# Performance work log

Hardware: AMD Instinct MI355X
Metric: run time of the kernel (lower is better)

## Reference

```python
import jax, jax.numpy as jnp
import numpy as np

D = 768
ED = 192  # d // 4
E = 8     # n_experts
K = 2     # top_k
B, H, W = 32, 32, 32
LN_EPS = 1e-5


def setup_inputs() -> dict:
    key = jax.random.key(0)
    ks = jax.random.split(key, 5)
    s = 0.02
    x = jax.random.normal(ks[0], (B, D, H, W), dtype=jnp.float32)
    Wr = jax.random.normal(ks[1], (E, D), dtype=jnp.float32) * s   # router: logits = tokens @ Wr.T
    W1 = jax.random.normal(ks[2], (E, D, ED), dtype=jnp.float32) * s  # gate proj (silu branch)
    W3 = jax.random.normal(ks[3], (E, D, ED), dtype=jnp.float32) * s  # linear branch
    W2 = jax.random.normal(ks[4], (E, ED, D), dtype=jnp.float32) * s  # down proj
    gamma = jnp.ones((D,), dtype=jnp.float32)
    beta = jnp.zeros((D,), dtype=jnp.float32)
    return {"x": x, "Wr": Wr, "W1": W1, "W3": W3, "W2": W2, "gamma": gamma, "beta": beta}


def _layernorm(y, gamma, beta):
    mu = jnp.mean(y, axis=-1, keepdims=True)
    var = jnp.mean(jnp.square(y - mu), axis=-1, keepdims=True)
    return (y - mu) * jax.lax.rsqrt(var + LN_EPS) * gamma + beta


def _moe_forward(x, Wr, W1, W3, W2, gamma, beta):
    b, c, h, w = x.shape
    tokens = x.transpose(0, 2, 3, 1).reshape(-1, c)        # [T, d]
    logits = tokens @ Wr.T                                  # [T, E]
    topk_v, topk_i = jax.lax.top_k(logits, K)               # [T, K]
    topk_w = jax.nn.softmax(topk_v, axis=-1)                # [T, K]
    # dense combine weights: zero for non-selected experts (same math as masked scatter)
    gates = jnp.sum(jax.nn.one_hot(topk_i, E, dtype=tokens.dtype) * topk_w[..., None], axis=1)  # [T, E]
    # SwiGLU per expert (forward uses silu(e[0](t)) * e[2](t), then e[3])
    hdn = jax.nn.silu(jnp.einsum('td,edh->teh', tokens, W1)) * jnp.einsum('td,edh->teh', tokens, W3)  # [T,E,ed]
    y = jnp.einsum('te,teh,ehd->td', gates, hdn, W2)        # combine: [T, d]
    out = _layernorm(y, gamma, beta) + tokens
    return out.reshape(b, h, w, c).transpose(0, 3, 1, 2)


def reference(x, Wr, W1, W3, W2, gamma, beta):
    return _moe_forward(x, Wr, W1, W3, W2, gamma, beta)
```

## Files before the change

### kernel.cpp

```cpp
#include <hip/hip_runtime.h>
#include <cstdint>
#include <cstddef>

#define T_TOK 32768
#define DM 768
#define EDIM 192
#define NEXP 8

typedef unsigned short u16;
typedef short bf16x8 __attribute__((ext_vector_type(8)));
typedef float f32x4 __attribute__((ext_vector_type(4)));
typedef u16 u16x8 __attribute__((ext_vector_type(8)));

__device__ __forceinline__ u16 f2bf(float f) {
  unsigned u = __float_as_uint(f);
  return (u16)((u + 0x7FFFu + ((u >> 16) & 1u)) >> 16);
}
__device__ __forceinline__ float bf2f(u16 u) {
  return __uint_as_float(((unsigned)u) << 16);
}

__device__ __forceinline__ void gld16(const void* g, void* l) {
  __builtin_amdgcn_global_load_lds(
      (const __attribute__((address_space(1))) unsigned int*)g,
      (__attribute__((address_space(3))) unsigned int*)l,
      16, 0, 0);
}

__device__ __forceinline__ bf16x8 frag_ld(const u16* lds, int row, int kb) {
  int ph = row * 128 + (kb ^ ((row & 7) << 4));
  return *(const bf16x8*)((const char*)lds + ph);
}

__global__ __launch_bounds__(256) void k_prep(
    const float* __restrict__ W1, const float* __restrict__ W3,
    const float* __restrict__ W2, u16* __restrict__ W1T,
    u16* __restrict__ W3T, u16* __restrict__ W2T)
{
  __shared__ __align__(16) float td[64][68];
  const int z = blockIdx.z;
  const int mat = z >> 3, e = z & 7;
  const int R = (mat == 2) ? EDIM : DM;
  const int C = (mat == 2) ? DM : EDIM;
  const int r0 = blockIdx.x * 64, c0 = blockIdx.y * 64;
  if (r0 >= R || c0 >= C) return;
  const float* in = (mat == 0 ? W1 : mat == 1 ? W3 : W2) + (size_t)e * R * C;
  u16* out = (mat == 0 ? W1T : mat == 1 ? W3T : W2T) + (size_t)e * R * C;
  const int tid = threadIdx.x;
  {
    int rl = tid >> 2, cs = (tid & 3) * 16;
    const float* s = in + (size_t)(r0 + rl) * C + c0 + cs;
    #pragma unroll
    for (int i = 0; i < 16; i += 4) *(float4*)&td[rl][cs + i] = *(const float4*)(s + i);
  }
  __syncthreads();
  {
    int cl = tid >> 2, rs = (tid & 3) * 16;
    u16* d = out + (size_t)(c0 + cl) * R + r0 + rs;
    u16x8 o0, o1;
    #pragma unroll
    for (int i = 0; i < 8; ++i) {
      o0[i] = f2bf(td[rs + i][cl]);
      o1[i] = f2bf(td[rs + 8 + i][cl]);
    }
    *(u16x8*)d = o0;
    *(u16x8*)(d + 8) = o1;
  }
}

__global__ __launch_bounds__(256) void k_tokrouter(
    const float* __restrict__ x, const float* __restrict__ Wr,
    u16* __restrict__ tokbf, int* __restrict__ cnt,
    int* __restrict__ toklist, float* __restrict__ gatelist)
{
  __shared__ float WrL[8][772];
  __shared__ float xL[64][33];
  __shared__ float logitsL[32][8];
  __shared__ int cnt8[8];
  __shared__ int baseL[8];
  const int tid = threadIdx.x;
  const int t0 = blockIdx.x * 32;
  const int b = t0 >> 10;
  const int h = (t0 >> 5) & 31;
  const float* xb = x + (size_t)b * (DM * 1024) + h * 32;

  for (int i = tid; i < 1536; i += 256) {
    int r = i / 192;
    int c = (i - r * 192) * 4;
    *(float4*)&WrL[r][c] = ((const float4*)Wr)[i];
  }

  const int rt = tid >> 3;
  const int re = tid & 7;
  float lacc = 0.f;

  for (int cb = 0; cb < 12; ++cb) {
    const int c0 = cb * 64;
    __syncthreads();
    #pragma unroll
    for (int it = 0; it < 2; ++it) {
      int idx = it * 256 + tid;
      int r = idx >> 3, cc = (idx & 7) * 4;
      float4 v = *(const float4*)(xb + (size_t)(c0 + r) * 1024 + cc);
      xL[r][cc] = v.x; xL[r][cc + 1] = v.y; xL[r][cc + 2] = v.z; xL[r][cc + 3] = v.w;
    }
    __syncthreads();
    {
      const float* wr = &WrL[re][c0];
      #pragma unroll
      for (int c = 0; c < 64; ++c) lacc = fmaf(xL[c][rt], wr[c], lacc);
    }
    {
      u16x8 o;
      #pragma unroll
      for (int i = 0; i < 8; ++i) o[i] = f2bf(xL[re * 8 + i][rt]);
      *(u16x8*)(tokbf + (size_t)(t0 + rt) * DM + c0 + re * 8) = o;
    }
  }

  logitsL[rt][re] = lacc;
  if (tid < 8) cnt8[tid] = 0;
  __syncthreads();

  int e0 = -1, e1 = -1, lp0 = 0, lp1 = 0;
  float g0 = 0.f, g1 = 0.f;
  if (tid < 32) {
    float v0 = -1e30f, v1 = -1e30f;
    #pragma unroll
    for (int e = 0; e < 8; ++e) { float v = logitsL[tid][e]; if (v > v0) { v0 = v; e0 = e; } }
    #pragma unroll
    for (int e = 0; e < 8; ++e) {
      if (e == e0) continue;
      float v = logitsL[tid][e]; if (v > v1) { v1 = v; e1 = e; }
    }
    float w = expf(v1 - v0);
    g0 = 1.f / (1.f + w);
    g1 = w / (1.f + w);
    lp0 = atomicAdd(&cnt8[e0], 1);
    lp1 = atomicAdd(&cnt8[e1], 1);
  }
  __syncthreads();
  if (tid < 8) baseL[tid] = atomicAdd(&cnt[tid], cnt8[tid]);
  __syncthreads();
  if (tid < 32) {
    int tg = t0 + tid;
    int p0 = baseL[e0] + lp0;
    int p1 = baseL[e1] + lp1;
    toklist[e0 * T_TOK + p0] = tg;
    gatelist[e0 * T_TOK + p0] = g0;
    toklist[e1 * T_TOK + p1] = tg | (1 << 16);
    gatelist[e1 * T_TOK + p1] = g1;
  }
}

__global__ void k_prefix(const int* __restrict__ cnt, int* __restrict__ offs) {
  if (threadIdx.x == 0) {
    int s = 0;
    for (int e = 0; e < NEXP; ++e) { offs[e] = s; s += cnt[e]; }
    offs[NEXP] = s;
  }
}

__global__ __launch_bounds__(256) void k_ffn1(
    const u16* __restrict__ tokbf, const u16* __restrict__ W1T,
    const u16* __restrict__ W3T, const int* __restrict__ cnt,
    const int* __restrict__ offs, const int* __restrict__ toklist,
    u16* __restrict__ hbuf)
{
  __shared__ __align__(16) u16 As[128 * 64];
  __shared__ __align__(16) u16 B1s[64 * 64];
  __shared__ __align__(16) u16 B3s[64 * 64];
  __shared__ int rowbaseL[128];
  const int e = blockIdx.z;
  const int count = cnt[e];
  const int start = blockIdx.x * 128;
  if (start >= count) return;
  const int n0 = blockIdx.y * 64;
  const int rows = min(128, count - start);
  const int tid = threadIdx.x;

  if (tid < 128) {
    int r = (tid < rows) ? tid : 0;
    rowbaseL[tid] = (toklist[e * T_TOK + start + r] & 0xFFFF) * DM;
  }
  __syncthreads();

  const int lrow = tid >> 3;
  const int swq = (((tid & 7) * 16) ^ ((lrow & 7) << 4)) >> 1;
  const u16 *srcA[4], *srcB1[2], *srcB3[2];
  #pragma unroll
  for (int it = 0; it < 4; ++it)
    srcA[it] = tokbf + rowbaseL[it * 32 + lrow] + swq;
  #pragma unroll
  for (int it = 0; it < 2; ++it) {
    size_t wb = (size_t)(e * EDIM + n0 + it * 32 + lrow) * DM + swq;
    srcB1[it] = W1T + wb;
    srcB3[it] = W3T + wb;
  }

  const int w = tid >> 6, l = tid & 63;
  const int wm = (w >> 1) * 64, wn = (w & 1) * 32;
  const int lr = l & 15;
  const int lk = (l >> 4) * 16;

  f32x4 acc1[4][2], acc3[4][2];
  #pragma unroll
  for (int i = 0; i < 4; ++i)
    #pragma unroll
    for (int j = 0; j < 2; ++j) {
      acc1[i][j] = (f32x4){0.f, 0.f, 0.f, 0.f};
      acc3[i][j] = (f32x4){0.f, 0.f, 0.f, 0.f};
    }

  for (int kc = 0; kc < 12; ++kc) {
    const int ko = kc * 64;
    #pragma unroll
    for (int it = 0; it < 4; ++it)
      gld16(srcA[it] + ko, (char*)As + (it * 256 + tid) * 16);
    #pragma unroll
    for (int it = 0; it < 2; ++it) {
      gld16(srcB1[it] + ko, (char*)B1s + (it * 256 + tid) * 16);
      gld16(srcB3[it] + ko, (char*)B3s + (it * 256 + tid) * 16);
    }
    __syncthreads();
    #pragma unroll
    for (int kk = 0; kk < 2; ++kk) {
      const int kb = kk * 64 + lk;
      bf16x8 af[4], b1[2], b3[2];
      #pragma unroll
      for (int mf = 0; mf < 4; ++mf) af[mf] = frag_ld(As, wm + mf * 16 + lr, kb);
      #pragma unroll
      for (int nf = 0; nf < 2; ++nf) {
        b1[nf] = frag_ld(B1s, wn + nf * 16 + lr, kb);
        b3[nf] = frag_ld(B3s, wn + nf * 16 + lr, kb);
      }
      #pragma unroll
      for (int mf = 0; mf < 4; ++mf)
        #pragma unroll
        for (int nf = 0; nf < 2; ++nf) {
          acc1[mf][nf] = __builtin_amdgcn_mfma_f32_16x16x32_bf16(af[mf], b1[nf], acc1[mf][nf], 0, 0, 0);
          acc3[mf][nf] = __builtin_amdgcn_mfma_f32_16x16x32_bf16(af[mf], b3[nf], acc3[mf][nf], 0, 0, 0);
        }
    }
    __syncthreads();
  }

  const int rq = (l >> 4) * 4;
  const int abase = offs[e] + start;
  #pragma unroll
  for (int mf = 0; mf < 4; ++mf)
    #pragma unroll
    for (int nf = 0; nf < 2; ++nf)
      #pragma unroll
      for (int r = 0; r < 4; ++r) {
        int m = wm + mf * 16 + rq + r;
        if (m < rows) {
          float a = acc1[mf][nf][r];
          float hv = (a / (1.f + expf(-a))) * acc3[mf][nf][r];
          hbuf[(size_t)(abase + m) * EDIM + (n0 + wn + nf * 16 + lr)] = f2bf(hv);
        }
      }
}

__global__ __launch_bounds__(256) void k_ffn2(
    const u16* __restrict__ hbuf, const u16* __restrict__ W2T,
    const int* __restrict__ cnt, const int* __restrict__ offs,
    const int* __restrict__ toklist, const float* __restrict__ gatelist,
    u16* __restrict__ ypart)
{
  __shared__ __align__(16) u16 As[128 * 64];
  __shared__ __align__(16) u16 Bs[128 * 64];
  __shared__ int dstL[128];
  __shared__ float gL[128];
  const int e = blockIdx.z;
  const int count = cnt[e];
  const int start = blockIdx.x * 128;
  if (start >= count) return;
  const int n0 = blockIdx.y * 128;
  const int rows = min(128, count - start);
  const int tid = threadIdx.x;
  const int abase = offs[e] + start;

  if (tid < 128) {
    int r = (tid < rows) ? tid : 0;
    int entry = toklist[e * T_TOK + start + r];
    int t = entry & 0xFFFF, k = entry >> 16;
    dstL[tid] = (k * T_TOK + t) * DM;
    gL[tid] = gatelist[e * T_TOK + start + r];
  }
  __syncthreads();

  const int lrow = tid >> 3;
  const int swq = (((tid & 7) * 16) ^ ((lrow & 7) << 4)) >> 1;
  const u16 *srcA[4], *srcB[4];
  #pragma unroll
  for (int it = 0; it < 4; ++it) {
    int r = it * 32 + lrow;
    int rr = (r < rows) ? r : 0;
    srcA[it] = hbuf + (size_t)(abase + rr) * EDIM + swq;
    srcB[it] = W2T + (size_t)(e * DM + n0 + r) * EDIM + swq;
  }

  const int w = tid >> 6, l = tid & 63;
  const int wm = (w >> 1) * 64, wn = (w & 1) * 64;
  const int lr = l & 15;
  const int lk = (l >> 4) * 16;

  f32x4 acc[4][4];
  #pragma unroll
  for (int i = 0; i < 4; ++i)
    #pragma unroll
    for (int j = 0; j < 4; ++j) acc[i][j] = (f32x4){0.f, 0.f, 0.f, 0.f};

  for (int kc = 0; kc < 3; ++kc) {
    const int ko = kc * 64;
    #pragma unroll
    for (int it = 0; it < 4; ++it) {
      gld16(srcA[it] + ko, (char*)As + (it * 256 + tid) * 16);
      gld16(srcB[it] + ko, (char*)Bs + (it * 256 + tid) * 16);
    }
    __syncthreads();
    #pragma unroll
    for (int kk = 0; kk < 2; ++kk) {
      const int kb = kk * 64 + lk;
      bf16x8 af[4], bf_[4];
      #pragma unroll
      for (int mf = 0; mf < 4; ++mf) af[mf] = frag_ld(As, wm + mf * 16 + lr, kb);
      #pragma unroll
      for (int nf = 0; nf < 4; ++nf) bf_[nf] = frag_ld(Bs, wn + nf * 16 + lr, kb);
      #pragma unroll
      for (int mf = 0; mf < 4; ++mf)
        #pragma unroll
        for (int nf = 0; nf < 4; ++nf)
          acc[mf][nf] = __builtin_amdgcn_mfma_f32_16x16x32_bf16(af[mf], bf_[nf], acc[mf][nf], 0, 0, 0);
    }
    __syncthreads();
  }

  const int rq = (l >> 4) * 4;
  #pragma unroll
  for (int mf = 0; mf < 4; ++mf)
    #pragma unroll
    for (int nf = 0; nf < 4; ++nf)
      #pragma unroll
      for (int r = 0; r < 4; ++r) {
        int m = wm + mf * 16 + rq + r;
        if (m < rows) {
          float v = acc[mf][nf][r] * gL[m];
          ypart[(size_t)dstL[m] + (n0 + wn + nf * 16 + lr)] = f2bf(v);
        }
      }
}

__global__ __launch_bounds__(256) void k_stats(
    const u16* __restrict__ ypart, float* __restrict__ mu, float* __restrict__ rs)
{
  const int tid = threadIdx.x;
  const int t = blockIdx.x * 16 + (tid >> 4);
  const int j = tid & 15;
  const u16* y0 = ypart + (size_t)t * DM;
  const u16* y1 = y0 + (size_t)T_TOK * DM;
  float sum = 0.f, sq = 0.f;
  #pragma unroll
  for (int i = 0; i < 6; ++i) {
    int c = i * 128 + j * 8;
    u16x8 a = *(const u16x8*)(y0 + c);
    u16x8 b = *(const u16x8*)(y1 + c);
    #pragma unroll
    for (int q = 0; q < 8; ++q) {
      float v = bf2f(a[q]) + bf2f(b[q]);
      sum += v; sq += v * v;
    }
  }
  #pragma unroll
  for (int d = 1; d < 16; d <<= 1) { sum += __shfl_xor(sum, d); sq += __shfl_xor(sq, d); }
  if (j == 0) {
    float m = sum * (1.f / 768.f);
    float var = sq * (1.f / 768.f) - m * m;
    mu[t] = m;
    rs[t] = 1.f / sqrtf(var + 1e-5f);
  }
}

__global__ __launch_bounds__(256) void k_apply(
    const u16* __restrict__ ypart, const float* __restrict__ x,
    const float* __restrict__ gamma, const float* __restrict__ beta,
    const float* __restrict__ mu, const float* __restrict__ rs,
    float* __restrict__ out)
{
  __shared__ float lnT[64][65];
  const int tid = threadIdx.x;
  const int t0 = blockIdx.x * 64;
  const int c0 = blockIdx.y * 64;
  const int b = t0 >> 10;
  const int h0 = (t0 >> 5) & 31;
  const u16* y0 = ypart;
  const u16* y1 = ypart + (size_t)T_TOK * DM;
  {
    const int tl = tid >> 2, q = tid & 3;
    const size_t tbase = (size_t)(t0 + tl) * DM;
    const int c = c0 + q * 16;
    const float mu_ = mu[t0 + tl], rs_ = rs[t0 + tl];
    u16x8 a0 = *(const u16x8*)(y0 + tbase + c);
    u16x8 a1 = *(const u16x8*)(y0 + tbase + c + 8);
    u16x8 b0 = *(const u16x8*)(y1 + tbase + c);
    u16x8 b1 = *(const u16x8*)(y1 + tbase + c + 8);
    #pragma unroll
    for (int i = 0; i < 8; ++i) {
      float v = bf2f(a0[i]) + bf2f(b0[i]);
      lnT[q * 16 + i][tl] = (v - mu_) * rs_ * gamma[c + i] + beta[c + i];
      float u = bf2f(a1[i]) + bf2f(b1[i]);
      lnT[q * 16 + 8 + i][tl] = (u - mu_) * rs_ * gamma[c + 8 + i] + beta[c + 8 + i];
    }
  }
  __syncthreads();
  {
    int cl = tid >> 2, ts = (tid & 3) * 16;
    int c = c0 + cl;
    int hh = h0 + (ts >> 5), ww = ts & 31;
    size_t oidx = (((size_t)b * DM + c) * 32 + hh) * 32 + ww;
    #pragma unroll
    for (int i = 0; i < 16; i += 4) {
      float4 xv = *(const float4*)(x + oidx + i);
      float4 ov;
      ov.x = lnT[cl][ts + i + 0] + xv.x;
      ov.y = lnT[cl][ts + i + 1] + xv.y;
      ov.z = lnT[cl][ts + i + 2] + xv.z;
      ov.w = lnT[cl][ts + i + 3] + xv.w;
      *(float4*)(out + oidx + i) = ov;
    }
  }
}

constexpr size_t OFF_TOK  = 0;
constexpr size_t OFF_W1T  = OFF_TOK + (size_t)T_TOK * DM * 2;
constexpr size_t OFF_W3T  = OFF_W1T + (size_t)NEXP * EDIM * DM * 2;
constexpr size_t OFF_W2T  = OFF_W3T + (size_t)NEXP * EDIM * DM * 2;
constexpr size_t OFF_H    = OFF_W2T + (size_t)NEXP * EDIM * DM * 2;
constexpr size_t OFF_YP   = OFF_H + (size_t)T_TOK * 2 * EDIM * 2;
constexpr size_t OFF_CNT  = OFF_YP + (size_t)2 * T_TOK * DM * 2;
constexpr size_t OFF_OFFS = OFF_CNT + 256;
constexpr size_t OFF_LIST = OFF_OFFS + 256;
constexpr size_t OFF_GATE = OFF_LIST + (size_t)NEXP * T_TOK * 4;
constexpr size_t OFF_MU   = OFF_GATE + (size_t)NEXP * T_TOK * 4;
constexpr size_t OFF_RS   = OFF_MU + (size_t)T_TOK * 4;

extern "C" void kernel_launch(void* const* d_in, const int* in_sizes, int n_in,
                              void* d_out, int out_size, void* d_ws, size_t ws_size,
                              hipStream_t stream) {
  const float* x     = (const float*)d_in[0];
  const float* Wr    = (const float*)d_in[1];
  const float* W1    = (const float*)d_in[2];
  const float* W3    = (const float*)d_in[3];
  const float* W2    = (const float*)d_in[4];
  const float* gamma = (const float*)d_in[5];
  const float* beta  = (const float*)d_in[6];
  float* out = (float*)d_out;
  char* ws = (char*)d_ws;

  u16* tokbf = (u16*)(ws + OFF_TOK);
  u16* W1T   = (u16*)(ws + OFF_W1T);
  u16* W3T   = (u16*)(ws + OFF_W3T);
  u16* W2T   = (u16*)(ws + OFF_W2T);
  u16* hbuf  = (u16*)(ws + OFF_H);
  u16* ypart = (u16*)(ws + OFF_YP);
  int* cnt   = (int*)(ws + OFF_CNT);
  int* offs  = (int*)(ws + OFF_OFFS);
  int* toklist = (int*)(ws + OFF_LIST);
  float* gatelist = (float*)(ws + OFF_GATE);
  float* muB = (float*)(ws + OFF_MU);
  float* rsB = (float*)(ws + OFF_RS);

  hipMemsetAsync(cnt, 0, 64, stream);
  hipLaunchKernelGGL(k_prep, dim3(12, 12, 24), dim3(256), 0, stream,
                     W1, W3, W2, W1T, W3T, W2T);
  hipLaunchKernelGGL(k_tokrouter, dim3(1024), dim3(256), 0, stream,
                     x, Wr, tokbf, cnt, toklist, gatelist);
  hipLaunchKernelGGL(k_prefix, dim3(1), dim3(64), 0, stream, cnt, offs);
  hipLaunchKernelGGL(k_ffn1, dim3(256, 3, 8), dim3(256), 0, stream,
                     tokbf, W1T, W3T, cnt, offs, toklist, hbuf);
  hipLaunchKernelGGL(k_ffn2, dim3(256, 6, 8), dim3(256), 0, stream,
                     hbuf, W2T, cnt, offs, toklist, gatelist, ypart);
  hipLaunchKernelGGL(k_stats, dim3(2048), dim3(256), 0, stream,
                     ypart, muB, rsB);
  hipLaunchKernelGGL(k_apply, dim3(512, 12), dim3(256), 0, stream,
                     ypart, x, gamma, beta, muB, rsB, out);
}
```

Before: 238.3 us.

## Double-buffer FFN GEMM loads, widen ffn1 tile to full N, streamline apply

Both expert GEMM kernels now use double-buffered LDS tiles, so the next K-chunk's global-to-LDS loads are issued while the current chunk is being multiplied. k_ffn1 also moves to 512 threads per block covering all 192 hidden columns, so each token tile is gathered once instead of three times. The larger LDS footprint (about 128KB per block) limits occupancy to one block per CU. k_apply now processes 128 channels per block with swizzled LDS and vectorized gamma/beta loads, and it adds the residual from the bf16 token copy instead of re-reading fp32 x, which adds bf16 rounding error to the residual.

Result: slower. 284.0 us (+19.1%).

```diff
diff --git a/kernel.cpp b/kernel.cpp
--- a/kernel.cpp
+++ b/kernel.cpp
@@ -161,21 +161,20 @@
   }
 }
 
-__global__ __launch_bounds__(256) void k_ffn1(
+__global__ __launch_bounds__(512) void k_ffn1(
     const u16* __restrict__ tokbf, const u16* __restrict__ W1T,
     const u16* __restrict__ W3T, const int* __restrict__ cnt,
     const int* __restrict__ offs, const int* __restrict__ toklist,
     u16* __restrict__ hbuf)
 {
-  __shared__ __align__(16) u16 As[128 * 64];
-  __shared__ __align__(16) u16 B1s[64 * 64];
-  __shared__ __align__(16) u16 B3s[64 * 64];
+  __shared__ __align__(16) u16 As[2][128 * 64];
+  __shared__ __align__(16) u16 B1s[2][192 * 64];
+  __shared__ __align__(16) u16 B3s[2][192 * 64];
   __shared__ int rowbaseL[128];
   const int e = blockIdx.z;
   const int count = cnt[e];
   const int start = blockIdx.x * 128;
   if (start >= count) return;
-  const int n0 = blockIdx.y * 64;
   const int rows = min(128, count - start);
   const int tid = threadIdx.x;
 
@@ -187,57 +186,63 @@
 
   const int lrow = tid >> 3;
   const int swq = (((tid & 7) * 16) ^ ((lrow & 7) << 4)) >> 1;
-  const u16 *srcA[4], *srcB1[2], *srcB3[2];
-  #pragma unroll
-  for (int it = 0; it < 4; ++it)
-    srcA[it] = tokbf + rowbaseL[it * 32 + lrow] + swq;
-  #pragma unroll
-  for (int it = 0; it < 2; ++it) {
-    size_t wb = (size_t)(e * EDIM + n0 + it * 32 + lrow) * DM + swq;
-    srcB1[it] = W1T + wb;
-    srcB3[it] = W3T + wb;
-  }
+  const u16* srcA0 = tokbf + rowbaseL[lrow] + swq;
+  const u16* srcA1 = tokbf + rowbaseL[64 + lrow] + swq;
+  const u16 *srcB1_[3], *srcB3_[3];
+  #pragma unroll
+  for (int it = 0; it < 3; ++it) {
+    size_t wb = (size_t)(e * EDIM + it * 64 + lrow) * DM + swq;
+    srcB1_[it] = W1T + wb;
+    srcB3_[it] = W3T + wb;
+  }
+  const int dOff = tid * 16;
+
+  auto stage = [&](int bb, int kc) {
+    const int ko = kc * 64;
+    gld16(srcA0 + ko, (char*)As[bb] + dOff);
+    gld16(srcA1 + ko, (char*)As[bb] + 8192 + dOff);
+    #pragma unroll
+    for (int it = 0; it < 3; ++it) {
+      gld16(srcB1_[it] + ko, (char*)B1s[bb] + it * 8192 + dOff);
+      gld16(srcB3_[it] + ko, (char*)B3s[bb] + it * 8192 + dOff);
+    }
+  };
 
   const int w = tid >> 6, l = tid & 63;
-  const int wm = (w >> 1) * 64, wn = (w & 1) * 32;
+  const int wm = (w >> 2) * 64, wn = (w & 3) * 48;
   const int lr = l & 15;
   const int lk = (l >> 4) * 16;
 
-  f32x4 acc1[4][2], acc3[4][2];
+  f32x4 acc1[4][3], acc3[4][3];
   #pragma unroll
   for (int i = 0; i < 4; ++i)
     #pragma unroll
-    for (int j = 0; j < 2; ++j) {
+    for (int j = 0; j < 3; ++j) {
       acc1[i][j] = (f32x4){0.f, 0.f, 0.f, 0.f};
       acc3[i][j] = (f32x4){0.f, 0.f, 0.f, 0.f};
     }
 
+  stage(0, 0);
+  __syncthreads();
+
   for (int kc = 0; kc < 12; ++kc) {
-    const int ko = kc * 64;
-    #pragma unroll
-    for (int it = 0; it < 4; ++it)
-      gld16(srcA[it] + ko, (char*)As + (it * 256 + tid) * 16);
-    #pragma unroll
-    for (int it = 0; it < 2; ++it) {
-      gld16(srcB1[it] + ko, (char*)B1s + (it * 256 + tid) * 16);
-      gld16(srcB3[it] + ko, (char*)B3s + (it * 256 + tid) * 16);
-    }
-    __syncthreads();
+    const int cur = kc & 1;
+    if (kc < 11) stage(cur ^ 1, kc + 1);
     #pragma unroll
     for (int kk = 0; kk < 2; ++kk) {
       const int kb = kk * 64 + lk;
-      bf16x8 af[4], b1[2], b3[2];
-      #pragma unroll
-      for (int mf = 0; mf < 4; ++mf) af[mf] = frag_ld(As, wm + mf * 16 + lr, kb);
-      #pragma unroll
-      for (int nf = 0; nf < 2; ++nf) {
-        b1[nf] = frag_ld(B1s, wn + nf * 16 + lr, kb);
-        b3[nf] = frag_ld(B3s, wn + nf * 16 + lr, kb);
+      bf16x8 af[4], b1[3], b3[3];
+      #pragma unroll
+      for (int mf = 0; mf < 4; ++mf) af[mf] = frag_ld(As[cur], wm + mf * 16 + lr, kb);
+      #pragma unroll
+      for (int nf = 0; nf < 3; ++nf) {
+        b1[nf] = frag_ld(B1s[cur], wn + nf * 16 + lr, kb);
+        b3[nf] = frag_ld(B3s[cur], wn + nf * 16 + lr, kb);
       }
       #pragma unroll
       for (int mf = 0; mf < 4; ++mf)
         #pragma unroll
-        for (int nf = 0; nf < 2; ++nf) {
+        for (int nf = 0; nf < 3; ++nf) {
           acc1[mf][nf] = __builtin_amdgcn_mfma_f32_16x16x32_bf16(af[mf], b1[nf], acc1[mf][nf], 0, 0, 0);
           acc3[mf][nf] = __builtin_amdgcn_mfma_f32_16x16x32_bf16(af[mf], b3[nf], acc3[mf][nf], 0, 0, 0);
         }
@@ -250,14 +255,14 @@
   #pragma unroll
   for (int mf = 0; mf < 4; ++mf)
     #pragma unroll
-    for (int nf = 0; nf < 2; ++nf)
+    for (int nf = 0; nf < 3; ++nf)
       #pragma unroll
       for (int r = 0; r < 4; ++r) {
         int m = wm + mf * 16 + rq + r;
         if (m < rows) {
           float a = acc1[mf][nf][r];
           float hv = (a / (1.f + expf(-a))) * acc3[mf][nf][r];
-          hbuf[(size_t)(abase + m) * EDIM + (n0 + wn + nf * 16 + lr)] = f2bf(hv);
+          hbuf[(size_t)(abase + m) * EDIM + (wn + nf * 16 + lr)] = f2bf(hv);
         }
       }
 }
@@ -268,8 +273,8 @@
     const int* __restrict__ toklist, const float* __restrict__ gatelist,
     u16* __restrict__ ypart)
 {
-  __shared__ __align__(16) u16 As[128 * 64];
-  __shared__ __align__(16) u16 Bs[128 * 64];
+  __shared__ __align__(16) u16 As[2][128 * 64];
+  __shared__ __align__(16) u16 Bs[2][128 * 64];
   __shared__ int dstL[128];
   __shared__ float gL[128];
   const int e = blockIdx.z;
@@ -300,6 +305,16 @@
     srcA[it] = hbuf + (size_t)(abase + rr) * EDIM + swq;
     srcB[it] = W2T + (size_t)(e * DM + n0 + r) * EDIM + swq;
   }
+  const int dOff = tid * 16;
+
+  auto stage = [&](int bb, int kc) {
+    const int ko = kc * 64;
+    #pragma unroll
+    for (int it = 0; it < 4; ++it) {
+      gld16(srcA[it] + ko, (char*)As[bb] + it * 4096 + dOff);
+      gld16(srcB[it] + ko, (char*)Bs[bb] + it * 4096 + dOff);
+    }
+  };
 
   const int w = tid >> 6, l = tid & 63;
   const int wm = (w >> 1) * 64, wn = (w & 1) * 64;
@@ -312,22 +327,20 @@
     #pragma unroll
     for (int j = 0; j < 4; ++j) acc[i][j] = (f32x4){0.f, 0.f, 0.f, 0.f};
 
+  stage(0, 0);
+  __syncthreads();
+
   for (int kc = 0; kc < 3; ++kc) {
-    const int ko = kc * 64;
-    #pragma unroll
-    for (int it = 0; it < 4; ++it) {
-      gld16(srcA[it] + ko, (char*)As + (it * 256 + tid) * 16);
-      gld16(srcB[it] + ko, (char*)Bs + (it * 256 + tid) * 16);
-    }
-    __syncthreads();
+    const int cur = kc & 1;
+    if (kc < 2) stage(cur ^ 1, kc + 1);
     #pragma unroll
     for (int kk = 0; kk < 2; ++kk) {
       const int kb = kk * 64 + lk;
       bf16x8 af[4], bf_[4];
       #pragma unroll
-      for (int mf = 0; mf < 4; ++mf) af[mf] = frag_ld(As, wm + mf * 16 + lr, kb);
-      #pragma unroll
-      for (int nf = 0; nf < 4; ++nf) bf_[nf] = frag_ld(Bs, wn + nf * 16 + lr, kb);
+      for (int mf = 0; mf < 4; ++mf) af[mf] = frag_ld(As[cur], wm + mf * 16 + lr, kb);
+      #pragma unroll
+      for (int nf = 0; nf < 4; ++nf) bf_[nf] = frag_ld(Bs[cur], wn + nf * 16 + lr, kb);
       #pragma unroll
       for (int mf = 0; mf < 4; ++mf)
         #pragma unroll
@@ -383,51 +396,60 @@
 }
 
 __global__ __launch_bounds__(256) void k_apply(
-    const u16* __restrict__ ypart, const float* __restrict__ x,
+    const u16* __restrict__ ypart, const u16* __restrict__ tokbf,
     const float* __restrict__ gamma, const float* __restrict__ beta,
     const float* __restrict__ mu, const float* __restrict__ rs,
     float* __restrict__ out)
 {
-  __shared__ float lnT[64][65];
+  __shared__ float lnT[128][65];
   const int tid = threadIdx.x;
   const int t0 = blockIdx.x * 64;
-  const int c0 = blockIdx.y * 64;
+  const int c0 = blockIdx.y * 128;
   const int b = t0 >> 10;
   const int h0 = (t0 >> 5) & 31;
   const u16* y0 = ypart;
   const u16* y1 = ypart + (size_t)T_TOK * DM;
   {
     const int tl = tid >> 2, q = tid & 3;
-    const size_t tbase = (size_t)(t0 + tl) * DM;
-    const int c = c0 + q * 16;
+    const int cq = c0 + q * 32;
+    const size_t tbase = (size_t)(t0 + tl) * DM + cq;
+    u16x8 a[4], bb[4], tk[4];
+    #pragma unroll
+    for (int i = 0; i < 4; ++i) {
+      a[i]  = *(const u16x8*)(y0 + tbase + i * 8);
+      bb[i] = *(const u16x8*)(y1 + tbase + i * 8);
+      tk[i] = *(const u16x8*)(tokbf + tbase + i * 8);
+    }
     const float mu_ = mu[t0 + tl], rs_ = rs[t0 + tl];
-    u16x8 a0 = *(const u16x8*)(y0 + tbase + c);
-    u16x8 a1 = *(const u16x8*)(y0 + tbase + c + 8);
-    u16x8 b0 = *(const u16x8*)(y1 + tbase + c);
-    u16x8 b1 = *(const u16x8*)(y1 + tbase + c + 8);
-    #pragma unroll
-    for (int i = 0; i < 8; ++i) {
-      float v = bf2f(a0[i]) + bf2f(b0[i]);
-      lnT[q * 16 + i][tl] = (v - mu_) * rs_ * gamma[c + i] + beta[c + i];
-      float u = bf2f(a1[i]) + bf2f(b1[i]);
-      lnT[q * 16 + 8 + i][tl] = (u - mu_) * rs_ * gamma[c + 8 + i] + beta[c + 8 + i];
+    const int colw = tl ^ ((q & 1) << 4);
+    #pragma unroll
+    for (int i = 0; i < 4; ++i) {
+      float4 g0 = *(const float4*)(gamma + cq + i * 8);
+      float4 g1 = *(const float4*)(gamma + cq + i * 8 + 4);
+      float4 b0 = *(const float4*)(beta + cq + i * 8);
+      float4 b1 = *(const float4*)(beta + cq + i * 8 + 4);
+      float gg[8] = {g0.x, g0.y, g0.z, g0.w, g1.x, g1.y, g1.z, g1.w};
+      float bt[8] = {b0.x, b0.y, b0.z, b0.w, b1.x, b1.y, b1.z, b1.w};
+      #pragma unroll
+      for (int u = 0; u < 8; ++u) {
+        float v = bf2f(a[i][u]) + bf2f(bb[i][u]);
+        lnT[q * 32 + i * 8 + u][colw] = (v - mu_) * rs_ * gg[u] + bt[u] + bf2f(tk[i][u]);
+      }
     }
   }
   __syncthreads();
   {
-    int cl = tid >> 2, ts = (tid & 3) * 16;
-    int c = c0 + cl;
-    int hh = h0 + (ts >> 5), ww = ts & 31;
-    size_t oidx = (((size_t)b * DM + c) * 32 + hh) * 32 + ww;
-    #pragma unroll
-    for (int i = 0; i < 16; i += 4) {
-      float4 xv = *(const float4*)(x + oidx + i);
+    const int cl = tid >> 1, half = tid & 1;
+    const int qx = (cl >> 5) & 1;
+    const size_t obase = (((size_t)b * DM + c0 + cl) * 32 + (h0 + half)) * 32;
+    #pragma unroll
+    for (int jj = 0; jj < 32; jj += 4) {
       float4 ov;
-      ov.x = lnT[cl][ts + i + 0] + xv.x;
-      ov.y = lnT[cl][ts + i + 1] + xv.y;
-      ov.z = lnT[cl][ts + i + 2] + xv.z;
-      ov.w = lnT[cl][ts + i + 3] + xv.w;
-      *(float4*)(out + oidx + i) = ov;
+      ov.x = lnT[cl][(half * 32 + jj + 0) ^ (qx << 4)];
+      ov.y = lnT[cl][(half * 32 + jj + 1) ^ (qx << 4)];
+      ov.z = lnT[cl][(half * 32 + jj + 2) ^ (qx << 4)];
+      ov.w = lnT[cl][(half * 32 + jj + 3) ^ (qx << 4)];
+      *(float4*)(out + obase + jj) = ov;
     }
   }
 }
@@ -477,12 +499,12 @@
   hipLaunchKernelGGL(k_tokrouter, dim3(1024), dim3(256), 0, stream,
                      x, Wr, tokbf, cnt, toklist, gatelist);
   hipLaunchKernelGGL(k_prefix, dim3(1), dim3(64), 0, stream, cnt, offs);
-  hipLaunchKernelGGL(k_ffn1, dim3(256, 3, 8), dim3(256), 0, stream,
+  hipLaunchKernelGGL(k_ffn1, dim3(256, 1, 8), dim3(512), 0, stream,
                      tokbf, W1T, W3T, cnt, offs, toklist, hbuf);
   hipLaunchKernelGGL(k_ffn2, dim3(256, 6, 8), dim3(256), 0, stream,
                      hbuf, W2T, cnt, offs, toklist, gatelist, ypart);
   hipLaunchKernelGGL(k_stats, dim3(2048), dim3(256), 0, stream,
                      ypart, muB, rsB);
-  hipLaunchKernelGGL(k_apply, dim3(512, 12), dim3(256), 0, stream,
-                     ypart, x, gamma, beta, muB, rsB, out);
-}
+  hipLaunchKernelGGL(k_apply, dim3(512, 6), dim3(256), 0, stream,
+                     ypart, tokbf, gamma, beta, muB, rsB, out);
+}
```
